# Optimization experiments

Hardware: AMD Instinct MI355X
Metric: run time of the kernel (lower is better)

The kernel has to match this reference:

```python
import jax, jax.numpy as jnp
import numpy as np

N, E, DX, DT, H, C = 100000, 1000000, 126, 2, 8, 16
F_IN = DX + DT          # 128
F_OUT = H * C           # 128
NEG_SLOPE = 0.2


def setup_inputs() -> dict:
    key = jax.random.key(0)
    ks = jax.random.split(key, 12)
    s = 1.0 / np.sqrt(F_IN)
    return {
        "x": jax.random.normal(ks[0], (N, DX), jnp.float32),
        "time_feat": jax.random.normal(ks[1], (N, DT), jnp.float32),
        "edge_index": jax.random.randint(ks[2], (2, E), 0, N, jnp.int64),
        "Wl": jax.random.normal(ks[3], (F_IN, F_OUT), jnp.float32) * s,
        "Wr": jax.random.normal(ks[4], (F_IN, F_OUT), jnp.float32) * s,
        "att": jax.random.normal(ks[5], (H, C), jnp.float32) * 0.25,
        "bias_gat": jax.random.normal(ks[6], (F_OUT,), jnp.float32) * 0.01,
        "Ws": jax.random.normal(ks[7], (F_IN, F_OUT), jnp.float32) * s,
        "bs": jax.random.normal(ks[8], (F_OUT,), jnp.float32) * 0.01,
        "Wo": jax.random.normal(ks[9], (F_OUT, 1), jnp.float32) * (1.0 / np.sqrt(F_OUT)),
        "bo": jax.random.normal(ks[10], (1,), jnp.float32) * 0.01,
    }


def reference(x, time_feat, edge_index, Wl, Wr, att, bias_gat, Ws, bs, Wo, bo):
    raw = jnp.concatenate([x, time_feat], axis=1)            # [N, F_IN]
    n = raw.shape[0]
    # PyG GATv2Conv adds self-loops by default
    loops = jnp.arange(n, dtype=edge_index.dtype)
    src = jnp.concatenate([edge_index[0], loops])             # [E+N]
    dst = jnp.concatenate([edge_index[1], loops])

    xl = (raw @ Wl).reshape(n, H, C)                          # source transform
    xr = (raw @ Wr).reshape(n, H, C)                          # target transform

    m = xl[src] + xr[dst]                                     # [E+N, H, C]
    e = jnp.einsum('ehc,hc->eh', jax.nn.leaky_relu(m, NEG_SLOPE), att)

    # segment softmax over incoming edges of each destination node
    emax = jax.ops.segment_max(e, dst, num_segments=n)        # [N, H]
    ee = jnp.exp(e - emax[dst])
    denom = jax.ops.segment_sum(ee, dst, num_segments=n)
    alpha = ee / (denom[dst] + 1e-16)                         # [E+N, H]

    agg = jax.ops.segment_sum(alpha[:, :, None] * xl[src], dst, num_segments=n)
    graph_x = agg.reshape(n, F_OUT) + bias_gat                # concat heads

    skip_x = raw @ Ws + bs
    combined = jax.nn.elu(graph_x + skip_x)
    return jax.nn.sigmoid(combined @ Wo + bo)                 # [N, 1]
```

## Files before the change

kernel.cpp:

```cpp
#include <hip/hip_runtime.h>
#include <hip/hip_bf16.h>

#define NEG_SLOPE 0.2f
#define LOG2E 1.4426950408889634f

typedef __bf16 v8bf __attribute__((ext_vector_type(8)));
typedef float  v4f  __attribute__((ext_vector_type(4)));

static __device__ __forceinline__ unsigned short f2b(float f) {
    unsigned u = __builtin_bit_cast(unsigned, f);
    u += 0x7FFFu + ((u >> 16) & 1u);
    return (unsigned short)(u >> 16);
}
static __device__ __forceinline__ void b2f2(unsigned u, float& lo, float& hi) {
    lo = __builtin_bit_cast(float, u << 16);
    hi = __builtin_bit_cast(float, u & 0xFFFF0000u);
}
static __device__ __forceinline__ void unpack8(uint4 u, float* f) {
    b2f2(u.x, f[0], f[1]); b2f2(u.y, f[2], f[3]);
    b2f2(u.z, f[4], f[5]); b2f2(u.w, f[6], f[7]);
}
static __device__ __forceinline__ int atomIncI(int* p) {
    return __hip_atomic_fetch_add(p, 1, __ATOMIC_RELAXED, __HIP_MEMORY_SCOPE_AGENT);
}

__global__ __launch_bounds__(256) void kA_prep(
    const float* __restrict__ Wl, const float* __restrict__ Wr,
    const float* __restrict__ Ws, unsigned short* __restrict__ Wt,
    int* __restrict__ zero_region, int nzero)
{
    int b = blockIdx.x;
    if (b < 192) {
        int t = b * 256 + threadIdx.x;
        int nn = t >> 7, k = t & 127;
        const float* W = (nn < 128) ? Wl : ((nn < 256) ? Wr : Ws);
        Wt[t] = f2b(W[k * 128 + (nn & 127)]);
    } else {
        int t = (b - 192) * 256 + threadIdx.x;
        if (t < nzero) zero_region[t] = 0;
    }
}

#define KB_HB 512

__global__ __launch_bounds__(256) void kB_hist_gemm(
    const int* __restrict__ ei, int E,
    int* __restrict__ counts, int* __restrict__ rank,
    const float* __restrict__ x, const float* __restrict__ tf,
    const unsigned short* __restrict__ Wt,
    const float* __restrict__ bg, const float* __restrict__ bs,
    unsigned short* __restrict__ xl_b, unsigned short* __restrict__ xr_b,
    unsigned short* __restrict__ sk_b, int N)
{
    __shared__ unsigned short lds[12672];
    const int tid = threadIdx.x;

    if (blockIdx.x < KB_HB) {
        const int stride = KB_HB * 256;
        for (int e = blockIdx.x * 256 + tid; e < E; e += stride) {
            int dst = ei[E + e];
            rank[e] = atomIncI(&counts[dst]);
        }
        return;
    }

    const int tb = (int)blockIdx.x - KB_HB;
    const int base = tb * 32;

    #pragma unroll
    for (int t = 0; t < 8; ++t) {
        int idx = tid + t * 256;
        if (idx < 2016) {
            int row = idx / 63;
            int c = idx - row * 63;
            int gr = base + row; if (gr >= N) gr = N - 1;
            float2 v = *reinterpret_cast<const float2*>(x + (size_t)gr * 126 + 2 * c);
            unsigned u = (unsigned)f2b(v.x) | ((unsigned)f2b(v.y) << 16);
            *reinterpret_cast<unsigned*>(&lds[row * 136 + 2 * c]) = u;
        }
    }
    if (tid < 32) {
        int gr = base + tid; if (gr >= N) gr = N - 1;
        float2 v = *reinterpret_cast<const float2*>(tf + (size_t)gr * 2);
        unsigned u = (unsigned)f2b(v.x) | ((unsigned)f2b(v.y) << 16);
        *reinterpret_cast<unsigned*>(&lds[tid * 136 + 126]) = u;
    }
    __syncthreads();

    const int wv = tid >> 6;
    const int lane = tid & 63;
    const int nidx = lane & 15, quad = lane >> 4;
    const int fbase = wv * 96;

    v4f acc[6][2];
    #pragma unroll
    for (int a = 0; a < 6; ++a)
        #pragma unroll
        for (int b = 0; b < 2; ++b) acc[a][b] = 0.0f;

    #pragma unroll
    for (int ks = 0; ks < 4; ++ks) {
        v8bf bfr[2];
        #pragma unroll
        for (int nf = 0; nf < 2; ++nf)
            bfr[nf] = *reinterpret_cast<const v8bf*>(
                &lds[(nf * 16 + nidx) * 136 + ks * 32 + quad * 8]);
        #pragma unroll
        for (int ft = 0; ft < 6; ++ft) {
            v8bf afr = *reinterpret_cast<const v8bf*>(
                Wt + (size_t)(fbase + ft * 16 + nidx) * 128 + ks * 32 + quad * 8);
            #pragma unroll
            for (int nf = 0; nf < 2; ++nf)
                acc[ft][nf] = __builtin_amdgcn_mfma_f32_16x16x32_bf16(
                    afr, bfr[nf], acc[ft][nf], 0, 0, 0);
        }
    }

    __syncthreads();

    #pragma unroll
    for (int ft = 0; ft < 6; ++ft) {
        const int f = fbase + ft * 16;
        const int arr = f >> 7;
        const int colb = (f & 127) + quad * 4;
        float b0 = 0.0f, b1 = 0.0f, b2 = 0.0f, b3 = 0.0f;
        if (arr == 2) {
            float4 v1 = *reinterpret_cast<const float4*>(bs + (f & 127) + quad * 4);
            float4 v2 = *reinterpret_cast<const float4*>(bg + (f & 127) + quad * 4);
            b0 = v1.x + v2.x; b1 = v1.y + v2.y; b2 = v1.z + v2.z; b3 = v1.w + v2.w;
        }
        #pragma unroll
        for (int nf = 0; nf < 2; ++nf) {
            const int nloc = nf * 16 + nidx;
            v4f v = acc[ft][nf];
            uint2 p;
            p.x = (unsigned)f2b(v[0] + b0) | ((unsigned)f2b(v[1] + b1) << 16);
            p.y = (unsigned)f2b(v[2] + b2) | ((unsigned)f2b(v[3] + b3) << 16);
            *reinterpret_cast<uint2*>(&lds[arr * 4224 + nloc * 132 + colb]) = p;
        }
    }
    __syncthreads();

    #pragma unroll
    for (int it = 0; it < 6; ++it) {
        int i = tid + it * 256;
        int arr = i >> 9;
        int idx = i & 511;
        int nloc = idx >> 4;
        int colh = (idx & 15) * 8;
        int node = base + nloc;
        if (node < N) {
            uint4 v = *reinterpret_cast<const uint4*>(&lds[arr * 4224 + nloc * 132 + colh]);
            unsigned short* dp = (arr == 0) ? xl_b : ((arr == 1) ? xr_b : sk_b);
            *reinterpret_cast<uint4*>(dp + (size_t)node * 128 + colh) = v;
        }
    }
}

__global__ __launch_bounds__(256) void ks_a(
    const int* __restrict__ counts, int* __restrict__ partial, int N)
{
    __shared__ int s[256];
    int t = threadIdx.x, i = blockIdx.x * 256 + t;
    s[t] = (i < N) ? counts[i] : 0;
    __syncthreads();
    #pragma unroll
    for (int off = 128; off >= 1; off >>= 1) {
        if (t < off) s[t] += s[t + off];
        __syncthreads();
    }
    if (t == 0) partial[blockIdx.x] = s[0];
}

__global__ __launch_bounds__(1024) void ks_bc(
    const int* __restrict__ counts, const int* __restrict__ partial,
    int2* __restrict__ range, int N, int NB)
{
    __shared__ int sp[1024];
    __shared__ int sc[256];
    const int t = threadIdx.x;
    sp[t] = (t < NB) ? partial[t] : 0;
    __syncthreads();
    #pragma unroll
    for (int off = 1; off < 1024; off <<= 1) {
        int v = (t >= off) ? sp[t - off] : 0;
        __syncthreads();
        sp[t] += v;
        __syncthreads();
    }
    const int blockbase = (blockIdx.x == 0) ? 0 : sp[blockIdx.x - 1];

    const int i = blockIdx.x * 256 + (t & 255);
    int c = 0;
    if (t < 256) {
        c = (i < N) ? counts[i] : 0;
        sc[t] = c;
    }
    __syncthreads();
    #pragma unroll
    for (int off = 1; off < 256; off <<= 1) {
        int v = 0;
        if (t < 256 && t >= off) v = sc[t - off];
        __syncthreads();
        if (t < 256) sc[t] += v;
        __syncthreads();
    }
    if (t < 256 && i < N)
        range[i] = make_int2(blockbase + sc[t] - c, c);
}

__global__ __launch_bounds__(256) void kD_scatter(
    const int* __restrict__ ei, int E,
    const int2* __restrict__ range, const int* __restrict__ rank,
    int* __restrict__ sorted_src)
{
    int e = blockIdx.x * 256 + threadIdx.x;
    if (e < E) {
        int src = ei[e];
        int dst = ei[E + e];
        sorted_src[range[dst].x + rank[e]] = src;
    }
}

__global__ __launch_bounds__(256, 6) void k2_aggfin(
    const int2* __restrict__ range, const int* __restrict__ sorted_src,
    const unsigned short* __restrict__ xl_b,
    const unsigned short* __restrict__ xr_b,
    const unsigned short* __restrict__ sk_b,
    const float* __restrict__ att,
    const float* __restrict__ Wo, const float* __restrict__ bo,
    float* __restrict__ out, int N)
{
    const int node = (int)((blockIdx.x * (size_t)blockDim.x + threadIdx.x) >> 6);
    const int lane = threadIdx.x & 63;
    if (node >= N) return;
    const int j = lane & 15;
    const int g = lane >> 4;
    const int cb = j * 8;

    float4 a0 = *reinterpret_cast<const float4*>(att + cb);
    float4 a1 = *reinterpret_cast<const float4*>(att + cb + 4);
    float av[8] = {a0.x * LOG2E, a0.y * LOG2E, a0.z * LOG2E, a0.w * LOG2E,
                   a1.x * LOG2E, a1.y * LOG2E, a1.z * LOG2E, a1.w * LOG2E};
    float xr[8];
    unpack8(*reinterpret_cast<const uint4*>(xr_b + (size_t)node * 128 + cb), xr);

    float acc[8];
    #pragma unroll
    for (int c = 0; c < 8; ++c) acc[c] = 0.0f;
    float den = 0.0f;

    const int2 rc = range[node];
    const int total = rc.y + 1;
    const int srcbase = rc.x - 1;

    auto loadsrc = [&](int b0) -> int {
        int ii = b0 + g;
        int ic = (ii > 0 && ii < total) ? ii : 0;
        return (ic == 0) ? node : sorted_src[srcbase + ic];
    };
    auto gather = [&](int src) -> uint4 {
        return *reinterpret_cast<const uint4*>(xl_b + (size_t)src * 128 + cb);
    };

    int   sB = loadsrc(0);
    uint4 uA = gather(sB);
    sB = loadsrc(4);

    for (int b0 = 0; b0 < total; b0 += 4) {
        uint4 uB = gather(sB);
        int   sC = loadsrc(b0 + 8);

        bool valid = (b0 + g) < total;
        float xl[8];
        unpack8(uA, xl);
        float t = 0.0f;
        #pragma unroll
        for (int c = 0; c < 8; ++c) {
            float m = xl[c] + xr[c];
            float l = fmaxf(m, NEG_SLOPE * m);
            t = fmaf(l, av[c], t);
        }
        t += __shfl_xor(t, 1, 64);
        float e = valid ? exp2f(t) : 0.0f;
        #pragma unroll
        for (int c = 0; c < 8; ++c) acc[c] = fmaf(e, xl[c], acc[c]);
        den += e;

        uA = uB; sB = sC;
    }

    #pragma unroll
    for (int c = 0; c < 8; ++c) {
        acc[c] += __shfl_xor(acc[c], 16, 64);
        acc[c] += __shfl_xor(acc[c], 32, 64);
    }
    den += __shfl_xor(den, 16, 64);
    den += __shfl_xor(den, 32, 64);

    float rd = 1.0f / (den + 1e-16f);
    float sk[8];
    unpack8(*reinterpret_cast<const uint4*>(sk_b + (size_t)node * 128 + cb), sk);
    float4 w0 = *reinterpret_cast<const float4*>(Wo + cb);
    float4 w1 = *reinterpret_cast<const float4*>(Wo + cb + 4);
    float wv[8] = {w0.x, w0.y, w0.z, w0.w, w1.x, w1.y, w1.z, w1.w};
    float s = 0.0f;
    #pragma unroll
    for (int c = 0; c < 8; ++c) {
        float gg = fmaf(acc[c], rd, sk[c]);
        float el = gg > 0.0f ? gg : (exp2f(gg * LOG2E) - 1.0f);
        s = fmaf(el, wv[c], s);
    }
    s += __shfl_xor(s, 1, 64);
    s += __shfl_xor(s, 2, 64);
    s += __shfl_xor(s, 4, 64);
    s += __shfl_xor(s, 8, 64);
    if (lane == 0) {
        float z = s + bo[0];
        out[node] = 1.0f / (1.0f + exp2f(-z * LOG2E));
    }
}

extern "C" void kernel_launch(void* const* d_in, const int* in_sizes, int n_in,
                              void* d_out, int out_size, void* d_ws, size_t ws_size,
                              hipStream_t stream) {
    const float* x   = (const float*)d_in[0];
    const float* tf  = (const float*)d_in[1];
    const int*   ei  = (const int*)  d_in[2];
    const float* Wl  = (const float*)d_in[3];
    const float* Wr  = (const float*)d_in[4];
    const float* att = (const float*)d_in[5];
    const float* bg  = (const float*)d_in[6];
    const float* Ws  = (const float*)d_in[7];
    const float* bs  = (const float*)d_in[8];
    const float* Wo  = (const float*)d_in[9];
    const float* bo  = (const float*)d_in[10];
    float* out = (float*)d_out;

    const int N = in_sizes[0] / 126;
    const int E = in_sizes[2] / 2;
    const int NB = (N + 255) / 256;

    char* ws = (char*)d_ws;
    unsigned short* Wt   = (unsigned short*)ws; ws += (size_t)384 * 128 * 2;
    unsigned short* xl_b = (unsigned short*)ws; ws += (size_t)N * 128 * 2;
    unsigned short* xr_b = (unsigned short*)ws; ws += (size_t)N * 128 * 2;
    unsigned short* sk_b = (unsigned short*)ws; ws += (size_t)N * 128 * 2;
    int*  counts   = (int*)ws;  ws += (size_t)N * 4;
    int*  partial  = (int*)ws;  ws += (size_t)1024 * 4;
    int2* range    = (int2*)ws; ws += (size_t)N * 8;
    int*  rank     = (int*)ws;  ws += (size_t)E * 4;
    int*  sorted_src = (int*)ws; ws += (size_t)E * 4;

    hipLaunchKernelGGL(kA_prep, dim3(192 + (N + 255) / 256), dim3(256), 0, stream,
                       Wl, Wr, Ws, Wt, counts, N);
    const int GB = (N + 31) / 32;
    hipLaunchKernelGGL(kB_hist_gemm, dim3(KB_HB + GB), dim3(256), 0, stream,
                       ei, E, counts, rank, x, tf, Wt, bg, bs,
                       xl_b, xr_b, sk_b, N);
    hipLaunchKernelGGL(ks_a, dim3(NB), dim3(256), 0, stream, counts, partial, N);
    hipLaunchKernelGGL(ks_bc, dim3(NB), dim3(1024), 0, stream,
                       counts, partial, range, N, NB);
    hipLaunchKernelGGL(kD_scatter, dim3((E + 255) / 256), dim3(256), 0, stream,
                       ei, E, range, rank, sorted_src);
    hipLaunchKernelGGL(k2_aggfin, dim3((N + 3) / 4), dim3(256), 0, stream,
                       range, sorted_src, xl_b, xr_b, sk_b,
                       att, Wo, bo, out, N);
}
```

Before: 280.6 us.

## Split histogram from GEMM kernel and slice scatter by destination range

The fused histogram-plus-GEMM kernel is split into two separate launches: a one-edge-per-thread atomic histogram and a standalone bf16 GEMM. The CSR scatter now runs 8 passes over the edges, each writing only destinations in one eighth of the node range, so writes land in a smaller window of sorted_src that may fit in L2/MALL. The cost is reading the edge list 8 times and an extra kernel launch, and the histogram no longer overlaps with the GEMM.

```diff
diff --git a/kernel.cpp b/kernel.cpp
--- a/kernel.cpp
+++ b/kernel.cpp
@@ -41,11 +41,15 @@
     }
 }
 
-#define KB_HB 512
-
-__global__ __launch_bounds__(256) void kB_hist_gemm(
+__global__ __launch_bounds__(256) void kH_hist(
     const int* __restrict__ ei, int E,
-    int* __restrict__ counts, int* __restrict__ rank,
+    int* __restrict__ counts, int* __restrict__ rank)
+{
+    int e = blockIdx.x * 256 + threadIdx.x;
+    if (e < E) rank[e] = atomIncI(&counts[ei[E + e]]);
+}
+
+__global__ __launch_bounds__(256) void kG_gemm(
     const float* __restrict__ x, const float* __restrict__ tf,
     const unsigned short* __restrict__ Wt,
     const float* __restrict__ bg, const float* __restrict__ bs,
@@ -54,18 +58,7 @@
 {
     __shared__ unsigned short lds[12672];
     const int tid = threadIdx.x;
-
-    if (blockIdx.x < KB_HB) {
-        const int stride = KB_HB * 256;
-        for (int e = blockIdx.x * 256 + tid; e < E; e += stride) {
-            int dst = ei[E + e];
-            rank[e] = atomIncI(&counts[dst]);
-        }
-        return;
-    }
-
-    const int tb = (int)blockIdx.x - KB_HB;
-    const int base = tb * 32;
+    const int base = blockIdx.x * 32;
 
     #pragma unroll
     for (int t = 0; t < 8; ++t) {
@@ -209,16 +202,25 @@
         range[i] = make_int2(blockbase + sc[t] - c, c);
 }
 
+#define KD_EPT 8
 __global__ __launch_bounds__(256) void kD_scatter(
     const int* __restrict__ ei, int E,
     const int2* __restrict__ range, const int* __restrict__ rank,
-    int* __restrict__ sorted_src)
-{
-    int e = blockIdx.x * 256 + threadIdx.x;
-    if (e < E) {
-        int src = ei[e];
-        int dst = ei[E + e];
-        sorted_src[range[dst].x + rank[e]] = src;
+    int* __restrict__ sorted_src, int slice_sz)
+{
+    const int slice = blockIdx.x & 7;
+    const int chunk = blockIdx.x >> 3;
+    const int lo = slice * slice_sz;
+    const int hi = lo + slice_sz;
+    const int base = chunk * (256 * KD_EPT) + threadIdx.x;
+    #pragma unroll
+    for (int k = 0; k < KD_EPT; ++k) {
+        int e = base + k * 256;
+        if (e < E) {
+            int dst = ei[E + e];
+            if (dst >= lo && dst < hi)
+                sorted_src[range[dst].x + rank[e]] = ei[e];
+        }
     }
 }
 
@@ -354,15 +356,17 @@
 
     hipLaunchKernelGGL(kA_prep, dim3(192 + (N + 255) / 256), dim3(256), 0, stream,
                        Wl, Wr, Ws, Wt, counts, N);
-    const int GB = (N + 31) / 32;
-    hipLaunchKernelGGL(kB_hist_gemm, dim3(KB_HB + GB), dim3(256), 0, stream,
-                       ei, E, counts, rank, x, tf, Wt, bg, bs,
-                       xl_b, xr_b, sk_b, N);
+    hipLaunchKernelGGL(kH_hist, dim3((E + 255) / 256), dim3(256), 0, stream,
+                       ei, E, counts, rank);
+    hipLaunchKernelGGL(kG_gemm, dim3((N + 31) / 32), dim3(256), 0, stream,
+                       x, tf, Wt, bg, bs, xl_b, xr_b, sk_b, N);
     hipLaunchKernelGGL(ks_a, dim3(NB), dim3(256), 0, stream, counts, partial, N);
     hipLaunchKernelGGL(ks_bc, dim3(NB), dim3(1024), 0, stream,
                        counts, partial, range, N, NB);
-    hipLaunchKernelGGL(kD_scatter, dim3((E + 255) / 256), dim3(256), 0, stream,
-                       ei, E, range, rank, sorted_src);
+    const int slice_sz = (N + 7) / 8;
+    const int chunks = (E + 256 * KD_EPT - 1) / (256 * KD_EPT);
+    hipLaunchKernelGGL(kD_scatter, dim3(chunks * 8), dim3(256), 0, stream,
+                       ei, E, range, rank, sorted_src, slice_sz);
     hipLaunchKernelGGL(k2_aggfin, dim3((N + 3) / 4), dim3(256), 0, stream,
                        range, sorted_src, xl_b, xr_b, sk_b,
                        att, Wo, bo, out, N);
```

New measurement: 288.1 us. +2.7%, slower.
